# Kernel tuning notes

Hardware: AMD Instinct MI355X
Metric: run time of the kernel (lower is better)

The kernel has to match this reference:

```python
import jax, jax.numpy as jnp
import numpy as np

B, N, D = 2, 50000, 16
E = N * D  # total flattened neighbor entries


def setup_inputs() -> dict:
    key = jax.random.key(0)
    k1, k2, k3, k4 = jax.random.split(key, 4)
    xyz1 = jax.random.normal(k1, (B, N, 3), dtype=jnp.float32)
    # deformed coordinates = rest + small displacement (realistic ARAP setting)
    xyz2 = xyz1 + 0.1 * jax.random.normal(k2, (B, N, 3), dtype=jnp.float32)
    neighborList = jax.random.randint(k3, (E,), 0, N, dtype=jnp.int32)
    numNeighbors = jnp.full((N,), D, dtype=jnp.int32)
    accnumNeighbors = jnp.concatenate(
        [jnp.zeros((1,), jnp.int32), jnp.cumsum(numNeighbors)[:-1].astype(jnp.int32)])
    weightMatrix = jax.random.uniform(k4, (E,), dtype=jnp.float32)
    eye9 = jnp.eye(3, dtype=jnp.float32).reshape(9)
    rotations = jnp.broadcast_to(eye9, (B, N, 9))
    return {
        "xyz1": xyz1, "xyz2": xyz2, "neighborList": neighborList,
        "numNeighbors": numNeighbors, "accnumNeighbors": accnumNeighbors,
        "weightMatrix": weightMatrix, "rotations": rotations, "arapWeight": 1,
    }


def _arap_rotations(xyz1, xyz2, neighborList, numNeighbors, weightMatrix):
    b, n, _ = xyz1.shape
    e = neighborList.shape[0]
    # CSR segment ids: vertex id owning each flattened neighbor entry
    seg = jnp.repeat(jnp.arange(n, dtype=jnp.int32), numNeighbors, total_repeat_length=e)
    d1 = xyz1[:, seg] - xyz1[:, neighborList]   # [B,E,3] rest-pose edge vectors
    d2 = xyz2[:, seg] - xyz2[:, neighborList]   # [B,E,3] deformed edge vectors
    # weighted covariance contributions S_e = w_e * d1 d2^T : [B,E,3,3]
    outer = weightMatrix[None, :, None, None] * d1[..., :, None] * d2[..., None, :]
    # per-vertex covariance S_i = sum_{j in N(i)} S_e : [B,N,3,3]
    S = jax.vmap(lambda o: jax.ops.segment_sum(o, seg, num_segments=n))(outer)
    # Procrustes fit: R = V U^T with reflection fix
    U, s, Vt = jnp.linalg.svd(S)
    V = jnp.swapaxes(Vt, -1, -2)
    Ut = jnp.swapaxes(U, -1, -2)
    R = V @ Ut
    det = jnp.linalg.det(R)                      # [B,N]
    V = V.at[..., :, 2].multiply(jnp.where(det < 0, -1.0, 1.0)[..., None])
    R = V @ Ut
    return R.reshape(b, n, 9)


def reference(xyz1, xyz2, neighborList, numNeighbors, accnumNeighbors,
              weightMatrix, rotations, arapWeight):
    # accnumNeighbors (prefix offsets), rotations (initial guess) and arapWeight
    # are consumed by the CUDA kernel for addressing / loss weighting but do not
    # change the fitted rotations; the math is the ARAP local step below.
    return _arap_rotations(xyz1, xyz2, neighborList, numNeighbors, weightMatrix)
```

## Files before the change

### kernel.cpp

```cpp
#include <hip/hip_runtime.h>
#include <hip/hip_bf16.h>


__global__ __launch_bounds__(256)
void arap_rot_kernel(const float* __restrict__ xyz1,
                     const float* __restrict__ xyz2,
                     const int*   __restrict__ nbr,
                     const int*   __restrict__ num,
                     const int*   __restrict__ acc,
                     const float* __restrict__ wgt,
                     float*       __restrict__ out,
                     int B, int N)
{
    int t = blockIdx.x * blockDim.x + threadIdx.x;
    int total = B * N;
    if (t >= total) return;
    int b = t / N;
    int i = t - b * N;

    const float* x1 = xyz1 + (size_t)b * N * 3;
    const float* x2 = xyz2 + (size_t)b * N * 3;

    float p1x = x1[i * 3 + 0], p1y = x1[i * 3 + 1], p1z = x1[i * 3 + 2];
    float p2x = x2[i * 3 + 0], p2y = x2[i * 3 + 1], p2z = x2[i * 3 + 2];

    float Sxx = 0.f, Sxy = 0.f, Sxz = 0.f;
    float Syx = 0.f, Syy = 0.f, Syz = 0.f;
    float Szx = 0.f, Szy = 0.f, Szz = 0.f;

    int a0  = acc[i];
    int cnt = num[i];
#pragma unroll 4
    for (int k = 0; k < cnt; ++k) {
        int   e  = a0 + k;
        int   j  = nbr[e];
        float we = wgt[e];
        float d1x = p1x - x1[j * 3 + 0];
        float d1y = p1y - x1[j * 3 + 1];
        float d1z = p1z - x1[j * 3 + 2];
        float d2x = p2x - x2[j * 3 + 0];
        float d2y = p2y - x2[j * 3 + 1];
        float d2z = p2z - x2[j * 3 + 2];
        Sxx += we * d1x * d2x;  Sxy += we * d1x * d2y;  Sxz += we * d1x * d2z;
        Syx += we * d1y * d2x;  Syy += we * d1y * d2y;  Syz += we * d1y * d2z;
        Szx += we * d1z * d2x;  Szy += we * d1z * d2y;  Szz += we * d1z * d2z;
    }

    float n00 =  Sxx + Syy + Szz;
    float n01 =  Syz - Szy;
    float n02 =  Szx - Sxz;
    float n03 =  Sxy - Syx;
    float n11 =  Sxx - Syy - Szz;
    float n12 =  Sxy + Syx;
    float n13 =  Szx + Sxz;
    float n22 = -Sxx + Syy - Szz;
    float n23 =  Syz + Szy;
    float n33 = -Sxx - Syy + Szz;

    float fro2 = Sxx*Sxx + Sxy*Sxy + Sxz*Sxz
               + Syx*Syx + Syy*Syy + Syz*Syz
               + Szx*Szx + Szy*Szy + Szz*Szz;
    float s = 2.0f * sqrtf(fro2) + 1e-30f;

    float m00 = n00 + s, m01 = n01, m02 = n02, m03 = n03;
    float m11 = n11 + s, m12 = n12, m13 = n13;
    float m22 = n22 + s, m23 = n23;
    float m33 = n33 + s;

    {
        float inv = 1.0f / (m00 + m11 + m22 + m33);
        m00 *= inv; m01 *= inv; m02 *= inv; m03 *= inv;
        m11 *= inv; m12 *= inv; m13 *= inv;
        m22 *= inv; m23 *= inv; m33 *= inv;
    }

#pragma unroll
    for (int it = 0; it < 16; ++it) {
        float p00 = m00*m00 + m01*m01 + m02*m02 + m03*m03;
        float p01 = m00*m01 + m01*m11 + m02*m12 + m03*m13;
        float p02 = m00*m02 + m01*m12 + m02*m22 + m03*m23;
        float p03 = m00*m03 + m01*m13 + m02*m23 + m03*m33;
        float p11 = m01*m01 + m11*m11 + m12*m12 + m13*m13;
        float p12 = m01*m02 + m11*m12 + m12*m22 + m13*m23;
        float p13 = m01*m03 + m11*m13 + m12*m23 + m13*m33;
        float p22 = m02*m02 + m12*m12 + m22*m22 + m23*m23;
        float p23 = m02*m03 + m12*m13 + m22*m23 + m23*m33;
        float p33 = m03*m03 + m13*m13 + m23*m23 + m33*m33;
        float inv = 1.0f / (p00 + p11 + p22 + p33);
        m00 = p00 * inv; m01 = p01 * inv; m02 = p02 * inv; m03 = p03 * inv;
        m11 = p11 * inv; m12 = p12 * inv; m13 = p13 * inv;
        m22 = p22 * inv; m23 = p23 * inv;
        m33 = p33 * inv;
    }

    float qw = m00, qx = m01, qy = m02, qz = m03, best = m00;
    {
        bool g = m11 > best;
        qw = g ? m01 : qw; qx = g ? m11 : qx; qy = g ? m12 : qy; qz = g ? m13 : qz;
        best = g ? m11 : best;
        g = m22 > best;
        qw = g ? m02 : qw; qx = g ? m12 : qx; qy = g ? m22 : qy; qz = g ? m23 : qz;
        best = g ? m22 : best;
        g = m33 > best;
        qw = g ? m03 : qw; qx = g ? m13 : qx; qy = g ? m23 : qy; qz = g ? m33 : qz;
    }
    {
        float inv = rsqrtf(qw*qw + qx*qx + qy*qy + qz*qz);
        qw *= inv; qx *= inv; qy *= inv; qz *= inv;
    }

    float xx = qx*qx, yy = qy*qy, zz = qz*qz;
    float xy = qx*qy, xz = qx*qz, yz = qy*qz;
    float wx = qw*qx, wy = qw*qy, wz = qw*qz;

    float* o = out + (size_t)t * 9;
    o[0] = 1.f - 2.f*(yy + zz);
    o[1] = 2.f*(xy - wz);
    o[2] = 2.f*(xz + wy);
    o[3] = 2.f*(xy + wz);
    o[4] = 1.f - 2.f*(xx + zz);
    o[5] = 2.f*(yz - wx);
    o[6] = 2.f*(xz - wy);
    o[7] = 2.f*(yz + wx);
    o[8] = 1.f - 2.f*(xx + yy);
}

extern "C" void kernel_launch(void* const* d_in, const int* in_sizes, int n_in,
                              void* d_out, int out_size, void* d_ws, size_t ws_size,
                              hipStream_t stream) {
    const float* xyz1 = (const float*)d_in[0];
    const float* xyz2 = (const float*)d_in[1];
    const int*   nbr  = (const int*)  d_in[2];
    const int*   num  = (const int*)  d_in[3];
    const int*   acc  = (const int*)  d_in[4];
    const float* wgt  = (const float*)d_in[5];
    float* out = (float*)d_out;

    int N = in_sizes[3];
    int B = in_sizes[0] / (N * 3);
    int total = B * N;
    int block = 256;
    int grid = (total + block - 1) / block;
    arap_rot_kernel<<<grid, block, 0, stream>>>(xyz1, xyz2, nbr, num, acc, wgt,
                                                out, B, N);
}
```

Before: 99.31 us.

## Prepack xyz1/xyz2 into interleaved float4 pairs and vectorize neighbor loads

Adds a prepack kernel that interleaves rest and deformed coordinates into adjacent float4 pairs in workspace. Each neighbor gather then becomes two 16-byte loads within one 32-byte span, where before it was six scalar loads spread over two arrays. A fast path for exactly 16 aligned neighbors loads indices and weights as int4/float4 and fully unrolls the loop. The cost is an extra kernel launch plus a write and re-read of the packed buffer, and the kernel assumes the workspace is large enough.

```diff
diff --git a/kernel.cpp b/kernel.cpp
--- a/kernel.cpp
+++ b/kernel.cpp
@@ -3,8 +3,22 @@
 
 
 __global__ __launch_bounds__(256)
-void arap_rot_kernel(const float* __restrict__ xyz1,
-                     const float* __restrict__ xyz2,
+void prepack_kernel(const float* __restrict__ xyz1,
+                    const float* __restrict__ xyz2,
+                    float4* __restrict__ pk,
+                    int total)
+{
+    int t = blockIdx.x * blockDim.x + threadIdx.x;
+    if (t >= total) return;
+    float4 a, c;
+    a.x = xyz1[t * 3 + 0]; a.y = xyz1[t * 3 + 1]; a.z = xyz1[t * 3 + 2]; a.w = 0.f;
+    c.x = xyz2[t * 3 + 0]; c.y = xyz2[t * 3 + 1]; c.z = xyz2[t * 3 + 2]; c.w = 0.f;
+    pk[2 * (size_t)t + 0] = a;
+    pk[2 * (size_t)t + 1] = c;
+}
+
+__global__ __launch_bounds__(256)
+void arap_rot_kernel(const float4* __restrict__ pk,
                      const int*   __restrict__ nbr,
                      const int*   __restrict__ num,
                      const int*   __restrict__ acc,
@@ -18,11 +32,12 @@
     int b = t / N;
     int i = t - b * N;
 
-    const float* x1 = xyz1 + (size_t)b * N * 3;
-    const float* x2 = xyz2 + (size_t)b * N * 3;
+    const float4* base = pk + 2 * (size_t)b * N;
 
-    float p1x = x1[i * 3 + 0], p1y = x1[i * 3 + 1], p1z = x1[i * 3 + 2];
-    float p2x = x2[i * 3 + 0], p2y = x2[i * 3 + 1], p2z = x2[i * 3 + 2];
+    float4 P1 = base[2 * i + 0];
+    float4 P2 = base[2 * i + 1];
+    float p1x = P1.x, p1y = P1.y, p1z = P1.z;
+    float p2x = P2.x, p2y = P2.y, p2z = P2.z;
 
     float Sxx = 0.f, Sxy = 0.f, Sxz = 0.f;
     float Syx = 0.f, Syy = 0.f, Syz = 0.f;
@@ -30,20 +45,44 @@
 
     int a0  = acc[i];
     int cnt = num[i];
-#pragma unroll 4
-    for (int k = 0; k < cnt; ++k) {
-        int   e  = a0 + k;
-        int   j  = nbr[e];
-        float we = wgt[e];
-        float d1x = p1x - x1[j * 3 + 0];
-        float d1y = p1y - x1[j * 3 + 1];
-        float d1z = p1z - x1[j * 3 + 2];
-        float d2x = p2x - x2[j * 3 + 0];
-        float d2y = p2y - x2[j * 3 + 1];
-        float d2z = p2z - x2[j * 3 + 2];
-        Sxx += we * d1x * d2x;  Sxy += we * d1x * d2y;  Sxz += we * d1x * d2z;
-        Syx += we * d1y * d2x;  Syy += we * d1y * d2y;  Syz += we * d1y * d2z;
-        Szx += we * d1z * d2x;  Szy += we * d1z * d2y;  Szz += we * d1z * d2z;
+
+    if (cnt == 16 && (a0 & 3) == 0) {
+        const int4*   nb4 = (const int4*)(nbr + a0);
+        const float4* w4  = (const float4*)(wgt + a0);
+#pragma unroll
+        for (int c = 0; c < 4; ++c) {
+            int4   jj = nb4[c];
+            float4 ww = w4[c];
+            int js[4] = {jj.x, jj.y, jj.z, jj.w};
+            float ws[4] = {ww.x, ww.y, ww.z, ww.w};
+#pragma unroll
+            for (int u = 0; u < 4; ++u) {
+                int j = js[u];
+                float4 A = base[2 * j + 0];
+                float4 C = base[2 * j + 1];
+                float we = ws[u];
+                float d1x = p1x - A.x, d1y = p1y - A.y, d1z = p1z - A.z;
+                float d2x = p2x - C.x, d2y = p2y - C.y, d2z = p2z - C.z;
+                float w1x = we * d1x, w1y = we * d1y, w1z = we * d1z;
+                Sxx += w1x * d2x;  Sxy += w1x * d2y;  Sxz += w1x * d2z;
+                Syx += w1y * d2x;  Syy += w1y * d2y;  Syz += w1y * d2z;
+                Szx += w1z * d2x;  Szy += w1z * d2y;  Szz += w1z * d2z;
+            }
+        }
+    } else {
+        for (int k = 0; k < cnt; ++k) {
+            int   e  = a0 + k;
+            int   j  = nbr[e];
+            float we = wgt[e];
+            float4 A = base[2 * j + 0];
+            float4 C = base[2 * j + 1];
+            float d1x = p1x - A.x, d1y = p1y - A.y, d1z = p1z - A.z;
+            float d2x = p2x - C.x, d2y = p2y - C.y, d2z = p2z - C.z;
+            float w1x = we * d1x, w1y = we * d1y, w1z = we * d1z;
+            Sxx += w1x * d2x;  Sxy += w1x * d2y;  Sxz += w1x * d2z;
+            Syx += w1y * d2x;  Syy += w1y * d2y;  Syz += w1y * d2z;
+            Szx += w1z * d2x;  Szy += w1z * d2y;  Szz += w1z * d2z;
+        }
     }
 
     float n00 =  Sxx + Syy + Szz;
@@ -139,8 +178,12 @@
     int N = in_sizes[3];
     int B = in_sizes[0] / (N * 3);
     int total = B * N;
+
+    float4* pk = (float4*)d_ws;
+
     int block = 256;
     int grid = (total + block - 1) / block;
-    arap_rot_kernel<<<grid, block, 0, stream>>>(xyz1, xyz2, nbr, num, acc, wgt,
+    prepack_kernel<<<grid, block, 0, stream>>>(xyz1, xyz2, pk, total);
+    arap_rot_kernel<<<grid, block, 0, stream>>>(pk, nbr, num, acc, wgt,
                                                 out, B, N);
 }
```

New measurement: 94.70 us (median of 2 runs). -4.6%, faster.
